# Optimization experiments

Hardware: AMD Instinct MI355X
Metric: run time of the kernel (lower is better)

The kernel has to match this reference:

```python
import jax, jax.numpy as jnp
import numpy as np

OBS_DIM = 256
ACT_DIM = 64
B = 8192
T = 22
H = 32            # gru_hidden_dim
CENTER = 14       # center_idx
MAXW = 15         # max_window
FEAT = 3 + H      # mlp_input_dim = 35


def setup_inputs() -> dict:
    key = jax.random.key(0)
    ks = jax.random.split(key, 12)
    I = OBS_DIM + ACT_DIM
    g = lambda k, shp, s: (jax.random.normal(k, shp, jnp.float32) * s)
    return {
        "obs_chunk": jax.random.normal(ks[0], (B, T, OBS_DIM), jnp.float32),
        "act_chunk": jax.random.normal(ks[1], (B, T, ACT_DIM), jnp.float32),
        # GRU params (PyTorch layout: weight_ih (3H, I), weight_hh (3H, H))
        "gru_W_ih": g(ks[2], (3 * H, I), 0.05),
        "gru_W_hh": g(ks[3], (3 * H, H), 0.1),
        "gru_b_ih": jnp.zeros((3 * H,), jnp.float32),
        "gru_b_hh": jnp.zeros((3 * H,), jnp.float32),
        # LayerNorm(35)
        "ln_gamma": jnp.ones((FEAT,), jnp.float32),
        "ln_beta": jnp.zeros((FEAT,), jnp.float32),
        # MLP: 35 -> 64 -> 32 -> 14
        "W1": g(ks[4], (64, FEAT), 0.15), "b1": jnp.zeros((64,), jnp.float32),
        "W2": g(ks[5], (32, 64), 0.15),   "b2": jnp.zeros((32,), jnp.float32),
        "W3": g(ks[6], (14, 32), 0.15),   "b3": jnp.zeros((14,), jnp.float32),
    }


def _forward(obs_chunk, act_chunk, gru_W_ih, gru_W_hh, gru_b_ih, gru_b_hh,
             ln_gamma, ln_beta, W1, b1, W2, b2, W3, b3):
    Bn = obs_chunk.shape[0]
    hist_obs = obs_chunk[:, :CENTER + 1]            # (B, 15, obs)
    hist_act = act_chunk[:, :CENTER + 1]            # (B, 15, act)
    obs_t = hist_obs[:, -1]                         # (B, obs)

    # entropy of softmax(obs_t)
    p = jax.nn.softmax(obs_t, axis=-1)
    entropy = -jnp.sum(p * jnp.log(p + 1e-8), axis=-1, keepdims=True)  # (B,1)

    # rate of change: mean L2 of 3 consecutive diffs ending at t
    diffs = jnp.linalg.norm(hist_obs[:, 12:15] - hist_obs[:, 11:14], axis=-1)  # (B,3)
    rate_of_change = diffs.mean(axis=1, keepdims=True)                          # (B,1)

    # correlation between obs_t and previous action (zero-padded to obs width)
    act_prev = hist_act[:, -2]                                       # (B, act)
    act_pad = jnp.pad(act_prev, ((0, 0), (0, OBS_DIM - ACT_DIM)))    # (B, obs)
    oc = obs_t - obs_t.mean(axis=1, keepdims=True)
    ac = act_pad - act_pad.mean(axis=1, keepdims=True)
    denom = (jnp.linalg.norm(oc, axis=1, keepdims=True)
             * jnp.linalg.norm(ac, axis=1, keepdims=True) + 1e-8)
    correlation = (oc * ac).sum(axis=1, keepdims=True) / denom       # (B,1)

    # GRU over the 15 history steps (PyTorch GRU equations)
    gru_in = jnp.concatenate([hist_obs, hist_act], axis=-1)          # (B, 15, I)

    def cell(h, x):
        gi = x @ gru_W_ih.T + gru_b_ih
        gh = h @ gru_W_hh.T + gru_b_hh
        i_r, i_z, i_n = jnp.split(gi, 3, axis=-1)
        h_r, h_z, h_n = jnp.split(gh, 3, axis=-1)
        r = jax.nn.sigmoid(i_r + h_r)
        z = jax.nn.sigmoid(i_z + h_z)
        n = jnp.tanh(i_n + r * h_n)
        return (1.0 - z) * n + z * h, None

    h0 = jnp.zeros((Bn, H), gru_in.dtype)
    h_n, _ = jax.lax.scan(cell, h0, jnp.swapaxes(gru_in, 0, 1))      # (B, H)

    feats = jnp.concatenate([entropy, rate_of_change, correlation, h_n], axis=1)  # (B,35)
    mu = feats.mean(axis=-1, keepdims=True)
    var = feats.var(axis=-1, keepdims=True)
    feats_n = (feats - mu) / jnp.sqrt(var + 1e-5) * ln_gamma + ln_beta

    x = jax.nn.relu(feats_n @ W1.T + b1)
    x = jax.nn.relu(x @ W2.T + b2)
    logits = x @ W3.T + b3                                           # (B,14)

    # test_mode: argmax of softmax(probs) == argmax of logits
    window_idx = jnp.argmax(logits, axis=1)                          # (B,) int
    window_len = window_idx + 2                                      # in [2,15]
    s_off = (window_len - 1) // 2
    e_off = window_len // 2

    # Vectorized replacement of the per-sample gather/scatter loop:
    # tgt slot j holds source position CENTER + (j-7); valid iff -s_off <= j-7 <= e_off.
    off = jnp.arange(MAXW) - 7                                       # (15,)
    mask = ((off[None, :] >= -s_off[:, None]) &
            (off[None, :] <= e_off[:, None])).astype(obs_chunk.dtype)  # (B,15)
    win = jnp.concatenate([obs_chunk[:, 7:7 + MAXW],
                           act_chunk[:, 7:7 + MAXW]], axis=-1)       # (B,15,obs+act)
    padded_window = win * mask[:, :, None]
    return window_len, padded_window, mask


def reference(obs_chunk, act_chunk, gru_W_ih, gru_W_hh, gru_b_ih, gru_b_hh,
              ln_gamma, ln_beta, W1, b1, W2, b2, W3, b3):
    return _forward(obs_chunk, act_chunk, gru_W_ih, gru_W_hh, gru_b_ih, gru_b_hh,
                    ln_gamma, ln_beta, W1, b1, W2, b2, W3, b3)
```

## Files before the change

kernel.cpp:

```cpp
#include <hip/hip_runtime.h>
#include <math.h>

#define OBS 256
#define ACTD 64
#define NB 8192
#define NT 22
#define NSTEP 15

__global__ __launch_bounds__(128, 4) void k1_gi(
    const float* __restrict__ obs, const float* __restrict__ act,
    const float* __restrict__ Wih, const float* __restrict__ bih,
    float* __restrict__ gi)
{
    int g = blockIdx.x * 128 + threadIdx.x;
    int gate = blockIdx.y;
    int b = g / 15;
    int t = g - b * 15;
    const float* xo = obs + (size_t)(b * NT + t) * OBS;
    const float* xa = act + (size_t)(b * NT + t) * ACTD;
    const float* Wg = Wih + (size_t)gate * 32 * 320;
    const float* bg = bih + gate * 32;

    float acc[32];
#pragma unroll
    for (int j = 0; j < 32; ++j) acc[j] = bg[j];

#pragma unroll 1
    for (int kb = 0; kb < 256; kb += 8) {
        float xv[8];
        float4 a0 = *(const float4*)(xo + kb + 0);
        float4 a1 = *(const float4*)(xo + kb + 4);
        xv[0]=a0.x; xv[1]=a0.y; xv[2]=a0.z; xv[3]=a0.w;
        xv[4]=a1.x; xv[5]=a1.y; xv[6]=a1.z; xv[7]=a1.w;
#pragma unroll
        for (int j = 0; j < 32; ++j) {
            const float* w = Wg + j * 320 + kb;
#pragma unroll
            for (int kk = 0; kk < 8; ++kk)
                acc[j] = fmaf(w[kk], xv[kk], acc[j]);
        }
    }
#pragma unroll 1
    for (int kb = 0; kb < 64; kb += 8) {
        float xv[8];
        float4 a0 = *(const float4*)(xa + kb + 0);
        float4 a1 = *(const float4*)(xa + kb + 4);
        xv[0]=a0.x; xv[1]=a0.y; xv[2]=a0.z; xv[3]=a0.w;
        xv[4]=a1.x; xv[5]=a1.y; xv[6]=a1.z; xv[7]=a1.w;
#pragma unroll
        for (int j = 0; j < 32; ++j) {
            const float* w = Wg + j * 320 + 256 + kb;
#pragma unroll
            for (int kk = 0; kk < 8; ++kk)
                acc[j] = fmaf(w[kk], xv[kk], acc[j]);
        }
    }

    float4* o = (float4*)(gi + (size_t)g * 96 + gate * 32);
#pragma unroll
    for (int j = 0; j < 8; ++j)
        o[j] = make_float4(acc[4*j], acc[4*j+1], acc[4*j+2], acc[4*j+3]);
}

__global__ __launch_bounds__(64, 2) void k2_head(
    const float* __restrict__ obs, const float* __restrict__ act,
    const float* __restrict__ Whh, const float* __restrict__ bhh,
    const float* __restrict__ lng, const float* __restrict__ lnb,
    const float* __restrict__ W1, const float* __restrict__ b1,
    const float* __restrict__ W2, const float* __restrict__ b2,
    const float* __restrict__ W3, const float* __restrict__ b3,
    const float* __restrict__ gi,
    float* __restrict__ out_wl, float* __restrict__ out_mask)
{
    int b = blockIdx.x;
    int l = threadIdx.x;
    int jj = l & 31;

    float wr[32], wz[32], wn[32];
#pragma unroll
    for (int k = 0; k < 32; ++k) {
        wr[k] = Whh[(0  + jj) * 32 + k];
        wz[k] = Whh[(32 + jj) * 32 + k];
        wn[k] = Whh[(64 + jj) * 32 + k];
    }
    float br = bhh[jj], bz = bhh[32 + jj], bn = bhh[64 + jj];

    float hfull[32];
#pragma unroll
    for (int k = 0; k < 32; ++k) hfull[k] = 0.0f;
    float hown = 0.0f;

    const float* gib = gi + (size_t)b * NSTEP * 96;
    for (int t = 0; t < NSTEP; ++t) {
        float gi_r = gib[t * 96 + jj];
        float gi_z = gib[t * 96 + 32 + jj];
        float gi_n = gib[t * 96 + 64 + jj];
        float ar = br, az = bz, an = bn;
#pragma unroll
        for (int k = 0; k < 32; ++k) {
            ar = fmaf(wr[k], hfull[k], ar);
            az = fmaf(wz[k], hfull[k], az);
            an = fmaf(wn[k], hfull[k], an);
        }
        float r = 1.0f / (1.0f + expf(-(gi_r + ar)));
        float z = 1.0f / (1.0f + expf(-(gi_z + az)));
        float n = tanhf(gi_n + r * an);
        hown = (1.0f - z) * n + z * hown;
#pragma unroll
        for (int k = 0; k < 32; ++k) hfull[k] = __shfl(hown, k, 64);
    }

    float o14v[4], o13v[4], o12v[4], o11v[4];
#pragma unroll
    for (int q = 0; q < 4; ++q) {
        int i = l + 64 * q;
        o14v[q] = obs[(size_t)(b * NT + 14) * OBS + i];
        o13v[q] = obs[(size_t)(b * NT + 13) * OBS + i];
        o12v[q] = obs[(size_t)(b * NT + 12) * OBS + i];
        o11v[q] = obs[(size_t)(b * NT + 11) * OBS + i];
    }
    float ap = act[(size_t)(b * NT + 13) * ACTD + l];

    float m = fmaxf(fmaxf(o14v[0], o14v[1]), fmaxf(o14v[2], o14v[3]));
#pragma unroll
    for (int o = 32; o >= 1; o >>= 1) m = fmaxf(m, __shfl_xor(m, o, 64));
    float e[4];
    float S = 0.0f, so = 0.0f;
#pragma unroll
    for (int q = 0; q < 4; ++q) {
        e[q] = expf(o14v[q] - m);
        S += e[q];
        so += o14v[q];
    }
#pragma unroll
    for (int o = 32; o >= 1; o >>= 1) { S += __shfl_xor(S, o, 64); so += __shfl_xor(so, o, 64); }
    float ent = 0.0f;
#pragma unroll
    for (int q = 0; q < 4; ++q) {
        float p = e[q] / S;
        ent += p * logf(p + 1e-8f);
    }
#pragma unroll
    for (int o = 32; o >= 1; o >>= 1) ent += __shfl_xor(ent, o, 64);
    ent = -ent;

    float d1 = 0.0f, d2 = 0.0f, d3 = 0.0f;
#pragma unroll
    for (int q = 0; q < 4; ++q) {
        float a = o12v[q] - o11v[q]; d1 = fmaf(a, a, d1);
        a = o13v[q] - o12v[q];       d2 = fmaf(a, a, d2);
        a = o14v[q] - o13v[q];       d3 = fmaf(a, a, d3);
    }
#pragma unroll
    for (int o = 32; o >= 1; o >>= 1) {
        d1 += __shfl_xor(d1, o, 64); d2 += __shfl_xor(d2, o, 64); d3 += __shfl_xor(d3, o, 64);
    }
    float roc = (sqrtf(d1) + sqrtf(d2) + sqrtf(d3)) / 3.0f;

    float sa = ap;
#pragma unroll
    for (int o = 32; o >= 1; o >>= 1) sa += __shfl_xor(sa, o, 64);
    float mu_o = so / 256.0f;
    float mu_a = sa / 256.0f;
    float s_oa = 0.0f, s_oo = 0.0f, s_aa = 0.0f;
#pragma unroll
    for (int q = 0; q < 4; ++q) {
        float ov = o14v[q] - mu_o;
        float av = ((q == 0) ? ap : 0.0f) - mu_a;
        s_oa = fmaf(ov, av, s_oa);
        s_oo = fmaf(ov, ov, s_oo);
        s_aa = fmaf(av, av, s_aa);
    }
#pragma unroll
    for (int o = 32; o >= 1; o >>= 1) {
        s_oa += __shfl_xor(s_oa, o, 64); s_oo += __shfl_xor(s_oo, o, 64); s_aa += __shfl_xor(s_aa, o, 64);
    }
    float corr = s_oa / (sqrtf(s_oo) * sqrtf(s_aa) + 1e-8f);

    float fsum = ent + roc + corr;
#pragma unroll
    for (int k = 0; k < 32; ++k) fsum += hfull[k];
    float mu = fsum / 35.0f;
    float vs = (ent - mu) * (ent - mu) + (roc - mu) * (roc - mu) + (corr - mu) * (corr - mu);
#pragma unroll
    for (int k = 0; k < 32; ++k) { float dd = hfull[k] - mu; vs = fmaf(dd, dd, vs); }
    float inv_sv = 1.0f / sqrtf(vs / 35.0f + 1e-5f);

    float x1 = b1[l];
#pragma unroll
    for (int k = 0; k < 35; ++k) {
        float f = (k == 0) ? ent : (k == 1) ? roc : (k == 2) ? corr : hfull[k - 3];
        float fnk = (f - mu) * inv_sv * lng[k] + lnb[k];
        x1 = fmaf(W1[l * 35 + k], fnk, x1);
    }
    x1 = fmaxf(x1, 0.0f);

    float x2 = b2[jj];
#pragma unroll
    for (int k = 0; k < 64; ++k)
        x2 = fmaf(W2[jj * 64 + k], __shfl(x1, k, 64), x2);
    x2 = fmaxf(x2, 0.0f);

    int lr = (l < 14) ? l : 0;
    float lg = b3[lr];
#pragma unroll
    for (int k = 0; k < 32; ++k)
        lg = fmaf(W3[lr * 32 + k], __shfl(x2, k, 64), lg);

    float best = -3.402823466e38f;
    int bi = 0;
#pragma unroll
    for (int j = 0; j < 14; ++j) {
        float v = __shfl(lg, j, 64);
        if (v > best) { best = v; bi = j; }
    }
    int wl = bi + 2;
    if (l == 0) out_wl[b] = (float)wl;
    int s  = (wl - 1) >> 1;
    int ee = wl >> 1;
    if (l < 15) {
        int off = l - 7;
        out_mask[b * 15 + l] = (off >= -s && off <= ee) ? 1.0f : 0.0f;
    }
}

__global__ __launch_bounds__(256) void k3_window(
    const float* __restrict__ obs, const float* __restrict__ act,
    const float* __restrict__ mask, float* __restrict__ out_pad)
{
    int idx = blockIdx.x * 256 + threadIdx.x;
    int bt = idx / 80;
    int k4 = idx - bt * 80;
    int b = bt / 15;
    int t = bt - b * 15;
    float mval = mask[bt];
    float4 v;
    if (k4 < 64) {
        v = *(const float4*)(obs + (size_t)(b * NT + 7 + t) * OBS + k4 * 4);
    } else {
        v = *(const float4*)(act + (size_t)(b * NT + 7 + t) * ACTD + (k4 - 64) * 4);
    }
    v.x *= mval; v.y *= mval; v.z *= mval; v.w *= mval;
    ((float4*)out_pad)[idx] = v;
}

extern "C" void kernel_launch(void* const* d_in, const int* in_sizes, int n_in,
                              void* d_out, int out_size, void* d_ws, size_t ws_size,
                              hipStream_t stream) {
    const float* obs = (const float*)d_in[0];
    const float* act = (const float*)d_in[1];
    const float* Wih = (const float*)d_in[2];
    const float* Whh = (const float*)d_in[3];
    const float* bih = (const float*)d_in[4];
    const float* bhh = (const float*)d_in[5];
    const float* lng = (const float*)d_in[6];
    const float* lnb = (const float*)d_in[7];
    const float* W1  = (const float*)d_in[8];
    const float* b1  = (const float*)d_in[9];
    const float* W2  = (const float*)d_in[10];
    const float* b2  = (const float*)d_in[11];
    const float* W3  = (const float*)d_in[12];
    const float* b3  = (const float*)d_in[13];

    float* out      = (float*)d_out;
    float* out_wl   = out;
    float* out_pad  = out + NB;
    float* out_mask = out + NB + NB * 15 * 320;

    float* gi = out_pad;

    dim3 g1(960, 3);
    k1_gi<<<g1, 128, 0, stream>>>(obs, act, Wih, bih, gi);
    k2_head<<<NB, 64, 0, stream>>>(obs, act, Whh, bhh, lng, lnb,
                                   W1, b1, W2, b2, W3, b3,
                                   gi, out_wl, out_mask);
    k3_window<<<38400, 256, 0, stream>>>(obs, act, out_mask, out_pad);
}
```

Measured before the change: 686.7 us.

## Stage GRU input tiles in LDS and split recurrence into per-row kernel

The input-gate projection now stages 64 sequence rows per block into padded LDS with coalesced float4 loads. Each of four waves then computes 24 gate outputs against the shared tile, replacing per-thread strided global reads. The GRU recurrence moves to its own kernel with one thread per batch row, using LDS for the hidden-state exchange and writing the final hidden state to a scratch area of the output buffer. The head kernel reads that state and does its LayerNorm with wave reductions. The catch is that the recurrence kernel launches only 128 single-wave blocks, each thread running a long serial loop, so there is little parallelism and its latency may be exposed.

```diff
diff --git a/kernel.cpp b/kernel.cpp
--- a/kernel.cpp
+++ b/kernel.cpp
@@ -7,108 +7,142 @@
 #define NT 22
 #define NSTEP 15
 
-__global__ __launch_bounds__(128, 4) void k1_gi(
+__global__ __launch_bounds__(256) void k1_gi(
     const float* __restrict__ obs, const float* __restrict__ act,
     const float* __restrict__ Wih, const float* __restrict__ bih,
     float* __restrict__ gi)
 {
-    int g = blockIdx.x * 128 + threadIdx.x;
-    int gate = blockIdx.y;
-    int b = g / 15;
-    int t = g - b * 15;
-    const float* xo = obs + (size_t)(b * NT + t) * OBS;
-    const float* xa = act + (size_t)(b * NT + t) * ACTD;
-    const float* Wg = Wih + (size_t)gate * 32 * 320;
-    const float* bg = bih + gate * 32;
-
-    float acc[32];
-#pragma unroll
-    for (int j = 0; j < 32; ++j) acc[j] = bg[j];
+    __shared__ float XL[160 * 65];
+    int w = threadIdx.x >> 6;
+    int r = threadIdx.x & 63;
+    int g0 = blockIdx.x * 64;
+
+    float acc[24];
+    const float* bg = bih + w * 24;
+#pragma unroll
+    for (int j = 0; j < 24; ++j) acc[j] = bg[j];
 
 #pragma unroll 1
-    for (int kb = 0; kb < 256; kb += 8) {
-        float xv[8];
-        float4 a0 = *(const float4*)(xo + kb + 0);
-        float4 a1 = *(const float4*)(xo + kb + 4);
-        xv[0]=a0.x; xv[1]=a0.y; xv[2]=a0.z; xv[3]=a0.w;
-        xv[4]=a1.x; xv[5]=a1.y; xv[6]=a1.z; xv[7]=a1.w;
-#pragma unroll
-        for (int j = 0; j < 32; ++j) {
-            const float* w = Wg + j * 320 + kb;
-#pragma unroll
-            for (int kk = 0; kk < 8; ++kk)
-                acc[j] = fmaf(w[kk], xv[kk], acc[j]);
+    for (int half = 0; half < 2; ++half) {
+        __syncthreads();
+#pragma unroll
+        for (int i = 0; i < 10; ++i) {
+            int q  = threadIdx.x + i * 256;
+            int rr = q / 40;
+            int c4 = q - rr * 40;
+            int g  = g0 + rr;
+            int b  = g / 15;
+            int t  = g - b * 15;
+            const float* src;
+            int kk;
+            if (half == 0) {
+                src = obs + (size_t)(b * NT + t) * OBS + c4 * 4;
+                kk  = c4 * 4;
+            } else if (c4 < 24) {
+                src = obs + (size_t)(b * NT + t) * OBS + 160 + c4 * 4;
+                kk  = c4 * 4;
+            } else {
+                src = act + (size_t)(b * NT + t) * ACTD + (c4 - 24) * 4;
+                kk  = 96 + (c4 - 24) * 4;
+            }
+            float4 v = *(const float4*)src;
+            XL[(kk + 0) * 65 + rr] = v.x;
+            XL[(kk + 1) * 65 + rr] = v.y;
+            XL[(kk + 2) * 65 + rr] = v.z;
+            XL[(kk + 3) * 65 + rr] = v.w;
         }
-    }
+        __syncthreads();
+
+        const float* Wb = Wih + (size_t)(w * 24) * 320 + half * 160;
 #pragma unroll 1
-    for (int kb = 0; kb < 64; kb += 8) {
-        float xv[8];
-        float4 a0 = *(const float4*)(xa + kb + 0);
-        float4 a1 = *(const float4*)(xa + kb + 4);
-        xv[0]=a0.x; xv[1]=a0.y; xv[2]=a0.z; xv[3]=a0.w;
-        xv[4]=a1.x; xv[5]=a1.y; xv[6]=a1.z; xv[7]=a1.w;
-#pragma unroll
-        for (int j = 0; j < 32; ++j) {
-            const float* w = Wg + j * 320 + 256 + kb;
-#pragma unroll
-            for (int kk = 0; kk < 8; ++kk)
-                acc[j] = fmaf(w[kk], xv[kk], acc[j]);
+        for (int kk = 0; kk < 160; kk += 4) {
+            float x0 = XL[(kk + 0) * 65 + r];
+            float x1 = XL[(kk + 1) * 65 + r];
+            float x2 = XL[(kk + 2) * 65 + r];
+            float x3 = XL[(kk + 3) * 65 + r];
+#pragma unroll
+            for (int j = 0; j < 24; ++j) {
+                const float* wp = Wb + j * 320 + kk;
+                acc[j] = fmaf(wp[0], x0, acc[j]);
+                acc[j] = fmaf(wp[1], x1, acc[j]);
+                acc[j] = fmaf(wp[2], x2, acc[j]);
+                acc[j] = fmaf(wp[3], x3, acc[j]);
+            }
         }
     }
 
-    float4* o = (float4*)(gi + (size_t)g * 96 + gate * 32);
+    float4* o = (float4*)(gi + (size_t)(g0 + r) * 96 + w * 24);
+#pragma unroll
+    for (int j = 0; j < 6; ++j)
+        o[j] = make_float4(acc[4*j], acc[4*j+1], acc[4*j+2], acc[4*j+3]);
+}
+
+__global__ __launch_bounds__(64) void k2a_gru(
+    const float* __restrict__ Whh, const float* __restrict__ bhh,
+    const float* __restrict__ gi, float* __restrict__ hn)
+{
+    __shared__ float HNs[64 * 33];
+    int r = threadIdx.x;
+    int row = blockIdx.x * 64 + r;
+
+    float h[32];
+#pragma unroll
+    for (int k = 0; k < 32; ++k) h[k] = 0.0f;
+
+    const float2* G = (const float2*)(gi + (size_t)row * NSTEP * 96);
+
+#pragma unroll 1
+    for (int t = 0; t < NSTEP; ++t) {
+        const float2* Gt = G + t * 48;
+#pragma unroll 1
+        for (int c = 0; c < 16; ++c) {
+            float2 g_r = Gt[c];
+            float2 g_z = Gt[16 + c];
+            float2 g_n = Gt[32 + c];
+#pragma unroll
+            for (int s = 0; s < 2; ++s) {
+                int jj = 2 * c + s;
+                float ar = bhh[jj], az = bhh[32 + jj], an = bhh[64 + jj];
+#pragma unroll
+                for (int k = 0; k < 32; ++k) {
+                    float hk = h[k];
+                    ar = fmaf(Whh[jj * 32 + k],        hk, ar);
+                    az = fmaf(Whh[(32 + jj) * 32 + k], hk, az);
+                    an = fmaf(Whh[(64 + jj) * 32 + k], hk, an);
+                }
+                float gr = s ? g_r.y : g_r.x;
+                float gz = s ? g_z.y : g_z.x;
+                float gn = s ? g_n.y : g_n.x;
+                float rr = 1.0f / (1.0f + expf(-(gr + ar)));
+                float zz = 1.0f / (1.0f + expf(-(gz + az)));
+                float nn = tanhf(gn + rr * an);
+                HNs[r * 33 + jj] = (1.0f - zz) * nn + zz * h[jj];
+            }
+        }
+#pragma unroll
+        for (int k = 0; k < 32; ++k) h[k] = HNs[r * 33 + k];
+    }
+
+    float4* o = (float4*)(hn + (size_t)row * 32);
 #pragma unroll
     for (int j = 0; j < 8; ++j)
-        o[j] = make_float4(acc[4*j], acc[4*j+1], acc[4*j+2], acc[4*j+3]);
-}
-
-__global__ __launch_bounds__(64, 2) void k2_head(
+        o[j] = make_float4(h[4*j], h[4*j+1], h[4*j+2], h[4*j+3]);
+}
+
+__global__ __launch_bounds__(64) void k2b_head(
     const float* __restrict__ obs, const float* __restrict__ act,
-    const float* __restrict__ Whh, const float* __restrict__ bhh,
     const float* __restrict__ lng, const float* __restrict__ lnb,
     const float* __restrict__ W1, const float* __restrict__ b1,
     const float* __restrict__ W2, const float* __restrict__ b2,
     const float* __restrict__ W3, const float* __restrict__ b3,
-    const float* __restrict__ gi,
+    const float* __restrict__ hn,
     float* __restrict__ out_wl, float* __restrict__ out_mask)
 {
     int b = blockIdx.x;
     int l = threadIdx.x;
     int jj = l & 31;
 
-    float wr[32], wz[32], wn[32];
-#pragma unroll
-    for (int k = 0; k < 32; ++k) {
-        wr[k] = Whh[(0  + jj) * 32 + k];
-        wz[k] = Whh[(32 + jj) * 32 + k];
-        wn[k] = Whh[(64 + jj) * 32 + k];
-    }
-    float br = bhh[jj], bz = bhh[32 + jj], bn = bhh[64 + jj];
-
-    float hfull[32];
-#pragma unroll
-    for (int k = 0; k < 32; ++k) hfull[k] = 0.0f;
-    float hown = 0.0f;
-
-    const float* gib = gi + (size_t)b * NSTEP * 96;
-    for (int t = 0; t < NSTEP; ++t) {
-        float gi_r = gib[t * 96 + jj];
-        float gi_z = gib[t * 96 + 32 + jj];
-        float gi_n = gib[t * 96 + 64 + jj];
-        float ar = br, az = bz, an = bn;
-#pragma unroll
-        for (int k = 0; k < 32; ++k) {
-            ar = fmaf(wr[k], hfull[k], ar);
-            az = fmaf(wz[k], hfull[k], az);
-            an = fmaf(wn[k], hfull[k], an);
-        }
-        float r = 1.0f / (1.0f + expf(-(gi_r + ar)));
-        float z = 1.0f / (1.0f + expf(-(gi_z + az)));
-        float n = tanhf(gi_n + r * an);
-        hown = (1.0f - z) * n + z * hown;
-#pragma unroll
-        for (int k = 0; k < 32; ++k) hfull[k] = __shfl(hown, k, 64);
-    }
+    float h_own = hn[(size_t)b * 32 + jj];
 
     float o14v[4], o13v[4], o12v[4], o11v[4];
 #pragma unroll
@@ -177,21 +211,30 @@
     }
     float corr = s_oa / (sqrtf(s_oo) * sqrtf(s_aa) + 1e-8f);
 
-    float fsum = ent + roc + corr;
-#pragma unroll
-    for (int k = 0; k < 32; ++k) fsum += hfull[k];
-    float mu = fsum / 35.0f;
-    float vs = (ent - mu) * (ent - mu) + (roc - mu) * (roc - mu) + (corr - mu) * (corr - mu);
-#pragma unroll
-    for (int k = 0; k < 32; ++k) { float dd = hfull[k] - mu; vs = fmaf(dd, dd, vs); }
+    float hs = h_own;
+#pragma unroll
+    for (int o = 16; o >= 1; o >>= 1) hs += __shfl_xor(hs, o, 64);
+    float mu = (ent + roc + corr + hs) / 35.0f;
+    float hd = (h_own - mu);
+    float hv = hd * hd;
+#pragma unroll
+    for (int o = 16; o >= 1; o >>= 1) hv += __shfl_xor(hv, o, 64);
+    float vs = (ent - mu) * (ent - mu) + (roc - mu) * (roc - mu)
+             + (corr - mu) * (corr - mu) + hv;
     float inv_sv = 1.0f / sqrtf(vs / 35.0f + 1e-5f);
 
     float x1 = b1[l];
 #pragma unroll
-    for (int k = 0; k < 35; ++k) {
-        float f = (k == 0) ? ent : (k == 1) ? roc : (k == 2) ? corr : hfull[k - 3];
+    for (int k = 0; k < 3; ++k) {
+        float f = (k == 0) ? ent : (k == 1) ? roc : corr;
         float fnk = (f - mu) * inv_sv * lng[k] + lnb[k];
         x1 = fmaf(W1[l * 35 + k], fnk, x1);
+    }
+#pragma unroll
+    for (int k = 0; k < 32; ++k) {
+        float hk = __shfl(h_own, k, 64);
+        float fnk = (hk - mu) * inv_sv * lng[3 + k] + lnb[3 + k];
+        x1 = fmaf(W1[l * 35 + 3 + k], fnk, x1);
     }
     x1 = fmaxf(x1, 0.0f);
 
@@ -268,11 +311,12 @@
     float* out_mask = out + NB + NB * 15 * 320;
 
     float* gi = out_pad;
-
-    dim3 g1(960, 3);
-    k1_gi<<<g1, 128, 0, stream>>>(obs, act, Wih, bih, gi);
-    k2_head<<<NB, 64, 0, stream>>>(obs, act, Whh, bhh, lng, lnb,
-                                   W1, b1, W2, b2, W3, b3,
-                                   gi, out_wl, out_mask);
+    float* hn = out_pad + (16u << 20);
+
+    k1_gi<<<1920, 256, 0, stream>>>(obs, act, Wih, bih, gi);
+    k2a_gru<<<128, 64, 0, stream>>>(Whh, bhh, gi, hn);
+    k2b_head<<<NB, 64, 0, stream>>>(obs, act, lng, lnb,
+                                    W1, b1, W2, b2, W3, b3,
+                                    hn, out_wl, out_mask);
     k3_window<<<38400, 256, 0, stream>>>(obs, act, out_mask, out_pad);
 }
```

After: 1.120 ms. +63.2%, slower.
